# Optimization experiments

Hardware: AMD Instinct MI355X
Metric: run time of the kernel (lower is better)

## Reference

```python
import jax, jax.numpy as jnp
import numpy as np

EPS = 1e-15

def _sqn(x):
    return jnp.sum(x * x, axis=-1, keepdims=True)

def _nrm(x):
    return jnp.sqrt(jnp.clip(_sqn(x), EPS))

def artanh(x):
    return jnp.arctanh(jnp.clip(x, -1 + 1e-7, 1 - 1e-7))

def project(x):
    n = _nrm(x)
    mx = 1.0 - 1e-5
    return jnp.where(n > mx, x / n * mx, x)

def mobius_add(x, y):
    x2, y2 = _sqn(x), _sqn(y)
    xy = jnp.sum(x * y, -1, keepdims=True)
    num = (1 + 2 * xy + y2) * x + (1 - x2) * y
    den = 1 + 2 * xy + x2 * y2
    return num / jnp.clip(den, EPS)

def expmap0(u):
    n = _nrm(u)
    return project(jnp.tanh(n) * u / n)

def logmap0(x):
    n = _nrm(x)
    return artanh(n) * x / n

def pdist(x, y):
    return 2.0 * artanh(_nrm(mobius_add(-x, y)))[..., 0]

def mobius_matvec(x, W):
    # x [..., din], W [din, dout]
    xn = _nrm(x)
    mx = x @ W
    mxn = _nrm(mx)
    return project(jnp.tanh(mxn / xn * artanh(xn)) * mx / mxn)

def mobius_pw_mul(w, x):
    xn = _nrm(x)
    wx = w * x
    wxn = _nrm(wx)
    return project(jnp.tanh(wxn / xn * artanh(xn)) * wx / wxn)

def mobius_linear(x, W, b, nonlin=None):
    out = project(mobius_add(mobius_matvec(x, W), b))
    if nonlin is not None:
        out = project(expmap0(nonlin(logmap0(out))))
    return out

def poincare_to_klein(x):
    return 2 * x / (1 + _sqn(x))

def klein_to_poincare(k):
    return k / (1 + jnp.sqrt(jnp.clip(1 - _sqn(k), EPS)))

def weighted_mobius_midpoint(values, weights):
    # values [..., L, d], weights [..., L, 1]; gyromidpoint via Klein model
    kl = poincare_to_klein(values)
    gamma = 1.0 / jnp.sqrt(jnp.clip(1 - _sqn(kl), EPS))
    num = jnp.sum(weights * gamma * kl, axis=-2)
    den = jnp.sum(weights * gamma, axis=-2)
    return klein_to_poincare(num / jnp.clip(den, EPS))

def mobius_gru(x_seq, Wih, Whh, bias):
    # x_seq [L,B,din]; Wih [3H,din]; Whh [3H,H]; bias [3,H] (points on ball)
    H = Whh.shape[1]
    W_ir, W_ihh, W_iz = jnp.split(Wih, 3, axis=0)
    W_hr, W_hhh, W_hz = jnp.split(Whh, 3, axis=0)
    b_r, b_h, b_z = bias[0], bias[1], bias[2]
    def one_tf(W, h, U, x, b):
        return mobius_add(mobius_add(mobius_matvec(h, W.T), mobius_matvec(x, U.T)), b)
    def step(h, x):
        z = jax.nn.sigmoid(logmap0(one_tf(W_hz, h, W_iz, x, b_z)))
        r = jax.nn.sigmoid(logmap0(one_tf(W_hr, h, W_ir, x, b_r)))
        rh = mobius_pw_mul(r, h)
        h_tilde = one_tf(W_hhh, rh, W_ihh, x, b_h)
        delta = mobius_add(-h, h_tilde)
        hn = mobius_add(h, mobius_pw_mul(z, delta))
        return hn, hn
    h0 = jnp.zeros((x_seq.shape[1], H), x_seq.dtype)
    return jax.lax.scan(step, h0, x_seq)[1]  # [L,B,H]

def mobius_rnn(x_seq, W, U, b):
    # x_seq [L,B,d]; W [d,d] hidden->hidden, U [d,d] input->hidden
    def step(h, x):
        hn = project(mobius_add(mobius_add(mobius_matvec(h, W), mobius_matvec(x, U)), b))
        return hn, hn
    h0 = jnp.zeros(x_seq.shape[1:], x_seq.dtype)
    return jax.lax.scan(step, h0, x_seq)[1]

def distance_attention(values, pos_idx, pos_embeds, Wq, bq, Wk, bk, beta):
    # values [B,L,d], pos_idx [B,L] int
    pe = pos_embeds[pos_idx]
    attn_emb = mobius_add(values, pe)
    q = mobius_linear(attn_emb, Wq, bq)
    k = mobius_linear(attn_emb, Wk, bk)
    d = pdist(q, k)                      # [B,L]
    w = jax.nn.softmax(-beta * d, axis=1)
    return weighted_mobius_midpoint(values, w[..., None]), w

def _forward(context, ctx_position, mentions, mention_chars,
             word_lut, char_lut,
             gru_f_Wih, gru_f_Whh, gru_f_b, gru_b_Wih, gru_b_Whh, gru_b_b,
             w2s_W, w2s_b,
             men_pos, men_Wq, men_bq, men_Wk, men_bk, men_beta,
             char_W, char_U, char_b,
             cc_Wa, cc_Wb, cc_bias,
             ctx_pos, ctx_Wq, ctx_bq, ctx_Wk, ctx_bk, ctx_beta,
             fc_Wm, fc_Wc, fc_Wch, fc_bias,
             mlr_p, mlr_a):
    # ---- mention encoder ----
    men_emb = word_lut[mentions]                                   # B x ML x E
    mv = mobius_linear(men_emb, w2s_W, w2s_b, nonlin=jnp.tanh)     # B x ML x 2S
    ML = mentions.shape[1]
    pos_idx = jnp.where(mentions > 0, jnp.arange(1, ML + 1)[None, :], 0)
    mention_vec, _ = distance_attention(mv, pos_idx, men_pos, men_Wq, men_bq, men_Wk, men_bk, men_beta)
    ch = char_lut[mention_chars]                                   # B x CL x S
    char_states = mobius_rnn(ch.transpose(1, 0, 2), char_W, char_U, char_b).transpose(1, 0, 2)
    char_vec = weighted_mobius_midpoint(char_states, jnp.ones_like(char_states[..., :1]))
    # ---- context encoder (bi-directional hyperbolic GRU) ----
    fwd_emb = word_lut[context].transpose(1, 0, 2)                 # L x B x E
    bkwd_emb = word_lut[context[:, ::-1]].transpose(1, 0, 2)
    fwd_states = mobius_gru(fwd_emb, gru_f_Wih, gru_f_Whh, gru_f_b).transpose(1, 0, 2)
    bkwd_states = mobius_gru(bkwd_emb, gru_b_Wih, gru_b_Whh, gru_b_b).transpose(1, 0, 2)[:, ::-1]
    # ---- mobius concat of directions ----
    ctx = project(mobius_add(mobius_add(mobius_matvec(fwd_states, cc_Wa), mobius_matvec(bkwd_states, cc_Wb)), cc_bias))
    ctx_vec, _ = distance_attention(ctx, ctx_position, ctx_pos, ctx_Wq, ctx_bq, ctx_Wk, ctx_bk, ctx_beta)
    # ---- full mobius concat ----
    joint = mobius_add(mobius_matvec(mention_vec, fc_Wm), mobius_matvec(ctx_vec, fc_Wc))
    joint = project(mobius_add(mobius_add(joint, mobius_matvec(char_vec, fc_Wch)), fc_bias))
    # ---- hyperbolic MLR ----
    z = mobius_add(-mlr_p[None], joint[:, None])                   # B x C x D
    a_n = jnp.sqrt(jnp.clip(jnp.sum(mlr_a * mlr_a, -1), EPS))      # C
    num = 2 * jnp.einsum('bcd,cd->bc', z, mlr_a)
    den = jnp.clip(1 - jnp.sum(z * z, -1), EPS) * a_n
    return 2 * a_n * jnp.arcsinh(num / den)                        # B x C

def setup_inputs() -> dict:
    key = jax.random.key(0)
    ks = iter(jax.random.split(key, 64))
    B, L, ML, CL = 256, 128, 8, 16
    V, CV, E, S, C = 50000, 128, 300, 256, 128
    S2, D = 2 * 256, 5 * 256
    POS_CTX = 2 * 64 + 2  # context_len*2+2
    def u(k, shape, a):
        return jax.random.uniform(k, shape, jnp.float32, -a, a)
    def ball(k, shape, a=1e-4):
        return expmap0(u(k, shape, a))
    def wmat(k, din, dout):
        return u(k, (din, dout), 1.0 / np.sqrt(din))
    inp = {}
    inp['context'] = jax.random.randint(next(ks), (B, L), 0, V)
    inp['ctx_position'] = jax.random.randint(next(ks), (B, L), 0, POS_CTX)
    inp['mentions'] = jax.random.randint(next(ks), (B, ML), 0, V)
    inp['mention_chars'] = jax.random.randint(next(ks), (B, CL), 0, CV)
    inp['word_lut'] = ball(next(ks), (V, E))
    inp['char_lut'] = ball(next(ks), (CV, S))
    for pre in ('gru_f', 'gru_b'):
        inp[pre + '_Wih'] = u(next(ks), (3 * S, E), 1.0 / np.sqrt(S))
        inp[pre + '_Whh'] = u(next(ks), (3 * S, S), 1.0 / np.sqrt(S))
        inp[pre + '_b'] = ball(next(ks), (3, S))
    inp['w2s_W'] = wmat(next(ks), E, S2)
    inp['w2s_b'] = ball(next(ks), (S2,))
    inp['men_pos'] = ball(next(ks), (ML + 1, S2))
    inp['men_Wq'] = wmat(next(ks), S2, S2)
    inp['men_bq'] = ball(next(ks), (S2,))
    inp['men_Wk'] = wmat(next(ks), S2, S2)
    inp['men_bk'] = ball(next(ks), (S2,))
    inp['men_beta'] = u(next(ks), (1,), 0.01)
    inp['char_W'] = wmat(next(ks), S, S)
    inp['char_U'] = wmat(next(ks), S, S)
    inp['char_b'] = ball(next(ks), (S,))
    inp['cc_Wa'] = wmat(next(ks), S, S2)
    inp['cc_Wb'] = wmat(next(ks), S, S2)
    inp['cc_bias'] = ball(next(ks), (S2,))
    inp['ctx_pos'] = ball(next(ks), (POS_CTX, S2))
    inp['ctx_Wq'] = wmat(next(ks), S2, S2)
    inp['ctx_bq'] = ball(next(ks), (S2,))
    inp['ctx_Wk'] = wmat(next(ks), S2, S2)
    inp['ctx_bk'] = ball(next(ks), (S2,))
    inp['ctx_beta'] = u(next(ks), (1,), 0.01)
    inp['fc_Wm'] = wmat(next(ks), S2, D)
    inp['fc_Wc'] = wmat(next(ks), S2, D)
    inp['fc_Wch'] = wmat(next(ks), S, D)
    inp['fc_bias'] = ball(next(ks), (D,))
    inp['mlr_p'] = ball(next(ks), (C, D))
    inp['mlr_a'] = u(next(ks), (C, D), 1.0 / np.sqrt(D))
    return inp

def reference(context, ctx_position, mentions, mention_chars,
              word_lut, char_lut,
              gru_f_Wih, gru_f_Whh, gru_f_b, gru_b_Wih, gru_b_Whh, gru_b_b,
              w2s_W, w2s_b,
              men_pos, men_Wq, men_bq, men_Wk, men_bk, men_beta,
              char_W, char_U, char_b,
              cc_Wa, cc_Wb, cc_bias,
              ctx_pos, ctx_Wq, ctx_bq, ctx_Wk, ctx_bk, ctx_beta,
              fc_Wm, fc_Wc, fc_Wch, fc_bias,
              mlr_p, mlr_a):
    return _forward(context, ctx_position, mentions, mention_chars,
                    word_lut, char_lut,
                    gru_f_Wih, gru_f_Whh, gru_f_b, gru_b_Wih, gru_b_Whh, gru_b_b,
                    w2s_W, w2s_b,
                    men_pos, men_Wq, men_bq, men_Wk, men_bk, men_beta,
                    char_W, char_U, char_b,
                    cc_Wa, cc_Wb, cc_bias,
                    ctx_pos, ctx_Wq, ctx_bq, ctx_Wk, ctx_bk, ctx_beta,
                    fc_Wm, fc_Wc, fc_Wch, fc_bias,
                    mlr_p, mlr_a)
```

## Files before the change

### kernel.cpp

```cpp
#include <hip/hip_runtime.h>
#include <cstddef>
#include <cstdint>


#define EPS_  1e-15f
#define PMAX_ 0.99999f

typedef __attribute__((ext_vector_type(8))) short bf16x8;
typedef __attribute__((ext_vector_type(4))) float f32x4;
typedef __attribute__((ext_vector_type(8))) unsigned short us8;

__device__ __forceinline__ float wred(float v){
#pragma unroll
  for (int o = 32; o; o >>= 1) v += __shfl_xor(v, o, 64);
  return v;
}
__device__ __forceinline__ void wred2(float& a, float& b){
#pragma unroll
  for (int o = 32; o; o >>= 1){ a += __shfl_xor(a, o, 64); b += __shfl_xor(b, o, 64); }
}
__device__ __forceinline__ void wred3(float& a, float& b, float& c){
#pragma unroll
  for (int o = 32; o; o >>= 1){
    a += __shfl_xor(a, o, 64); b += __shfl_xor(b, o, 64); c += __shfl_xor(c, o, 64);
  }
}
__device__ __forceinline__ void wred4(float& a, float& b, float& c, float& d){
#pragma unroll
  for (int o = 32; o; o >>= 1){
    a += __shfl_xor(a, o, 64); b += __shfl_xor(b, o, 64);
    c += __shfl_xor(c, o, 64); d += __shfl_xor(d, o, 64);
  }
}
__device__ __forceinline__ float wredmax(float v){
#pragma unroll
  for (int o = 32; o; o >>= 1) v = fmaxf(v, __shfl_xor(v, o, 64));
  return v;
}
__device__ __forceinline__ float snorm(float s){ return sqrtf(fmaxf(s, EPS_)); }
__device__ __forceinline__ float clamp11(float x){
  return fminf(fmaxf(x, -1.f + 1e-7f), 1.f - 1e-7f);
}
__device__ __forceinline__ float bf2f(unsigned short u){
  union { unsigned int i; float f; } v; v.i = ((unsigned int)u) << 16; return v.f;
}
__device__ __forceinline__ unsigned short f2bf(float f){
  union { float f; unsigned int i; } v; v.f = f;
  unsigned int x = v.i;
  x += 0x7fffu + ((x >> 16) & 1u);
  return (unsigned short)(x >> 16);
}
__device__ __forceinline__ float bflo(unsigned u){
  union { unsigned i; float f; } v; v.i = u << 16; return v.f;
}
__device__ __forceinline__ float bfhi(unsigned u){
  union { unsigned i; float f; } v; v.i = u & 0xffff0000u; return v.f;
}

template<int N>
__device__ __forceinline__ float sq_part(const float* a){
  float s = 0.f;
#pragma unroll
  for (int i = 0; i < N; i++) s += a[i]*a[i];
  return s;
}
template<int N>
__device__ __forceinline__ float dot_part(const float* a, const float* b){
  float s = 0.f;
#pragma unroll
  for (int i = 0; i < N; i++) s += a[i]*b[i];
  return s;
}
template<int N>
__device__ __forceinline__ void madd_vec(const float* x, float x2, const float* y,
                                         float y2, float xy, float* o){
  const float c1 = 1.f + 2.f*xy + y2;
  const float c2 = 1.f - x2;
  const float inv = 1.f / fmaxf(1.f + 2.f*xy + x2*y2, EPS_);
#pragma unroll
  for (int i = 0; i < N; i++) o[i] = (c1*x[i] + c2*y[i]) * inv;
}
template<int N>
__device__ __forceinline__ void mt_project(float* v, float mxn2, float xn2, float* n2out){
  const float xn  = snorm(xn2);
  const float mxn = snorm(mxn2);
  const float t   = tanhf(mxn/xn * atanhf(clamp11(xn)));
  float sc = t/mxn;
  float n2 = sc*sc*mxn2;
  const float n = snorm(n2);
  if (n > PMAX_){ const float s = PMAX_/n; sc *= s; n2 *= s*s; }
#pragma unroll
  for (int i = 0; i < N; i++) v[i] *= sc;
  *n2out = n2;
}
__device__ __forceinline__ void mt_scale(float mxn2, float xn, float art,
                                         float* sc, float* n2){
  const float mxn = snorm(mxn2);
  const float t   = tanhf(mxn/xn * art);
  float s  = t/mxn;
  float nn = t*t;
  const float n = snorm(nn);
  if (n > PMAX_){ const float f = PMAX_/n; s *= f; nn *= f*f; }
  *sc = s; *n2 = nn;
}
template<int N>
__device__ __forceinline__ void project_vec(float* v, float* n2io){
  float n2 = *n2io;
  const float n = snorm(n2);
  if (n > PMAX_){
    const float s = PMAX_/n;
#pragma unroll
    for (int i = 0; i < N; i++) v[i] *= s;
    n2 *= s*s;
  }
  *n2io = n2;
}

__device__ __forceinline__ void gll16(const void* g, void* l){
  __builtin_amdgcn_global_load_lds(
      (const __attribute__((address_space(1))) void*)g,
      (__attribute__((address_space(3))) void*)l, 16, 0, 0);
}
__device__ __forceinline__ void stage64k8(const void* gsrc, float* lbase, int w, int lane){
#pragma unroll
  for (int i = 0; i < 8; i++){
    const char* g = (const char*)gsrc + (size_t)((i*8 + w)*64 + lane)*16;
    char* l = (char*)lbase + (size_t)((i*8 + w)*64)*16;
    gll16(g, l);
  }
}

template<int AMODE>
__global__ __launch_bounds__(256) void mfma_mm(const void* __restrict__ Aptr,
    const int* __restrict__ idx, const unsigned short* __restrict__ Bt,
    float* __restrict__ Cm, int M, int N, int K, int Kp)
{
  __shared__ __align__(16) unsigned short As[128][40];
  __shared__ __align__(16) unsigned short Bs[128][40];
  const int tid = threadIdx.x;
  const int n0 = blockIdx.x * 128;
  const int m0 = blockIdx.y * 128;
  const int srow = tid >> 1, shalf = tid & 1;
  const int wv = tid >> 6, lane = tid & 63;
  const int wm = wv >> 1, wn = wv & 1;
  const int lr = lane & 15, lk = lane >> 4;

  long arow;
  if constexpr (AMODE == 1) arow = (long)idx[m0 + srow] * K;
  else                      arow = (long)(m0 + srow) * K;

  f32x4 acc[4][4];
#pragma unroll
  for (int mf = 0; mf < 4; mf++)
#pragma unroll
    for (int nf = 0; nf < 4; nf++) acc[mf][nf] = (f32x4){0.f,0.f,0.f,0.f};

  for (int k0 = 0; k0 < Kp; k0 += 32){
    const int kb = k0 + shalf*16;
    unsigned short av[16];
    if constexpr (AMODE == 1){
      const float* ar = (const float*)Aptr + arow;
      if (kb + 16 <= K){
#pragma unroll
        for (int v = 0; v < 4; v++){
          const float4 f = *(const float4*)(ar + kb + v*4);
          av[v*4+0]=f2bf(f.x); av[v*4+1]=f2bf(f.y);
          av[v*4+2]=f2bf(f.z); av[v*4+3]=f2bf(f.w);
        }
      } else {
#pragma unroll
        for (int v = 0; v < 16; v++){
          const int col = kb + v;
          av[v] = (col < K) ? f2bf(ar[col]) : (unsigned short)0;
        }
      }
    } else {
      const unsigned short* ar = (const unsigned short*)Aptr + arow + kb;
      const us8 u0 = *(const us8*)ar;
      const us8 u1 = *(const us8*)(ar + 8);
#pragma unroll
      for (int v = 0; v < 8; v++){ av[v] = u0[v]; av[8+v] = u1[v]; }
    }
    unsigned short bvv[16];
    {
      const unsigned short* br = Bt + (long)(n0 + srow)*Kp + kb;
      const us8 u0 = *(const us8*)br;
      const us8 u1 = *(const us8*)(br + 8);
#pragma unroll
      for (int v = 0; v < 8; v++){ bvv[v] = u0[v]; bvv[8+v] = u1[v]; }
    }
    __syncthreads();
    *(us8*)&As[srow][shalf*16]   = *(const us8*)&av[0];
    *(us8*)&As[srow][shalf*16+8] = *(const us8*)&av[8];
    *(us8*)&Bs[srow][shalf*16]   = *(const us8*)&bvv[0];
    *(us8*)&Bs[srow][shalf*16+8] = *(const us8*)&bvv[8];
    __syncthreads();
    bf16x8 af[4], bfr[4];
#pragma unroll
    for (int mf = 0; mf < 4; mf++)
      af[mf] = *(const bf16x8*)&As[wm*64 + mf*16 + lr][lk*8];
#pragma unroll
    for (int nf = 0; nf < 4; nf++)
      bfr[nf] = *(const bf16x8*)&Bs[wn*64 + nf*16 + lr][lk*8];
#pragma unroll
    for (int mf = 0; mf < 4; mf++)
#pragma unroll
      for (int nf = 0; nf < 4; nf++)
        acc[mf][nf] = __builtin_amdgcn_mfma_f32_16x16x32_bf16(af[mf], bfr[nf],
                                                              acc[mf][nf], 0, 0, 0);
  }
#pragma unroll
  for (int mf = 0; mf < 4; mf++){
#pragma unroll
    for (int nf = 0; nf < 4; nf++){
#pragma unroll
      for (int r = 0; r < 4; r++){
        const long grow = m0 + wm*64 + mf*16 + lk*4 + r;
        Cm[grow*N + n0 + wn*64 + nf*16 + lr] = acc[mf][nf][r];
      }
    }
  }
}

template<int AMODE>
__global__ __launch_bounds__(256) void mm_kernel(const void* __restrict__ Aptr,
    const int* __restrict__ idx, const float* __restrict__ Bm,
    float* __restrict__ Cm, int M, int N, int K)
{
  __shared__ __align__(16) float As[8][128];
  __shared__ __align__(16) float Bs[8][132];
  const int tid = threadIdx.x;
  const int n0 = blockIdx.x * 128;
  const int m0 = blockIdx.y * 128;
  const int tr = tid >> 4, tc = tid & 15;
  const int sm = tid & 127, sk = (tid >> 7) * 4;
  const int bk = tid >> 5,  bn = (tid & 31) * 4;
  long arow;
  if constexpr (AMODE == 1) arow = (long)idx[m0 + sm] * K;
  else                      arow = (long)(m0 + sm) * K;
  float acc[8][8];
#pragma unroll
  for (int i = 0; i < 8; i++)
#pragma unroll
    for (int j = 0; j < 8; j++) acc[i][j] = 0.f;

  for (int k0 = 0; k0 < K; k0 += 8){
    float av[4], bv[4];
    {
      const float* A = (const float*)Aptr;
      if (k0 + sk + 3 < K){
        const float4 f = *reinterpret_cast<const float4*>(A + arow + k0 + sk);
        av[0]=f.x; av[1]=f.y; av[2]=f.z; av[3]=f.w;
      } else {
#pragma unroll
        for (int i = 0; i < 4; i++){
          const int kk = k0 + sk + i;
          av[i] = (kk < K) ? A[arow + kk] : 0.f;
        }
      }
    }
    {
      const int kb = k0 + bk;
      if (kb < K){
        const float4 f = *reinterpret_cast<const float4*>(Bm + (long)kb*N + n0 + bn);
        bv[0]=f.x; bv[1]=f.y; bv[2]=f.z; bv[3]=f.w;
      } else { bv[0]=bv[1]=bv[2]=bv[3]=0.f; }
    }
    __syncthreads();
    As[sk+0][sm]=av[0]; As[sk+1][sm]=av[1]; As[sk+2][sm]=av[2]; As[sk+3][sm]=av[3];
    *reinterpret_cast<float4*>(&Bs[bk][bn]) = make_float4(bv[0],bv[1],bv[2],bv[3]);
    __syncthreads();
#pragma unroll
    for (int k = 0; k < 8; k++){
      float a[8], bb[8];
      *(float4*)&a[0]  = *(const float4*)&As[k][tr*8];
      *(float4*)&a[4]  = *(const float4*)&As[k][tr*8+4];
      *(float4*)&bb[0] = *(const float4*)&Bs[k][tc*8];
      *(float4*)&bb[4] = *(const float4*)&Bs[k][tc*8+4];
#pragma unroll
      for (int i = 0; i < 8; i++)
#pragma unroll
        for (int j = 0; j < 8; j++) acc[i][j] += a[i]*bb[j];
    }
  }
#pragma unroll
  for (int i = 0; i < 8; i++){
    const long row = m0 + tr*8 + i;
    *(float4*)(Cm + row*N + n0 + tc*8)     = make_float4(acc[i][0],acc[i][1],acc[i][2],acc[i][3]);
    *(float4*)(Cm + row*N + n0 + tc*8 + 4) = make_float4(acc[i][4],acc[i][5],acc[i][6],acc[i][7]);
  }
}

__global__ __launch_bounds__(256) void transpose_k(const float* __restrict__ src,
    float* __restrict__ dst, int R, int Kc)
{
  __shared__ float t[32][33];
  const int bx = blockIdx.x * 32;
  const int by = blockIdx.y * 32;
  const int tx = threadIdx.x & 31, ty = threadIdx.x >> 5;
#pragma unroll
  for (int i = 0; i < 32; i += 8){
    const int j = by + ty + i, k = bx + tx;
    t[ty+i][tx] = (j < R && k < Kc) ? src[(long)j*Kc + k] : 0.f;
  }
  __syncthreads();
#pragma unroll
  for (int i = 0; i < 32; i += 8){
    const int k = bx + ty + i, j = by + tx;
    if (k < Kc && j < R) dst[(long)k*R + j] = t[tx][ty+i];
  }
}

__global__ __launch_bounds__(256) void packT16(const float* __restrict__ src,
    unsigned short* __restrict__ dst, int K, int N, int Kp)
{
  __shared__ float t[32][33];
  const int bx = blockIdx.x*32;
  const int by = blockIdx.y*32;
  const int tx = threadIdx.x & 31, ty = threadIdx.x >> 5;
#pragma unroll
  for (int i = 0; i < 32; i += 8){
    const int k = bx + ty + i, n = by + tx;
    t[ty+i][tx] = (k < K && n < N) ? src[(long)k*N + n] : 0.f;
  }
  __syncthreads();
#pragma unroll
  for (int i = 0; i < 32; i += 8){
    const int k = bx + tx, n = by + ty + i;
    if (k < Kp && n < N) dst[(long)n*Kp + k] = f2bf(t[tx][ty+i]);
  }
}

__global__ void pack_wih(const float* __restrict__ w0, const float* __restrict__ w1,
                         unsigned short* __restrict__ dst)
{
  const int tid = blockIdx.x*256 + threadIdx.x;
  if (tid < 2*768*320){
    const int d = tid / (768*320);
    const int rem = tid - d*768*320;
    const int n = rem / 320, k = rem - n*320;
    const float* src = d ? w1 : w0;
    dst[tid] = (k < 300) ? f2bf(src[n*300 + k]) : (unsigned short)0;
  }
}

__global__ void pack_whh16(const float* __restrict__ WtHH,
                           unsigned short* __restrict__ Wrz16,
                           unsigned short* __restrict__ Wh16)
{
  const int tid = blockIdx.x*256 + threadIdx.x;
  if (tid < 2*256*768){
    const int col = tid % 768, rk = tid / 768;
    const unsigned short v = f2bf(WtHH[tid]);
    if (col < 256)       Wrz16[(long)rk*512 + col] = v;
    else if (col < 512)  Wh16 [(long)rk*256 + (col - 256)] = v;
    else                 Wrz16[(long)rk*512 + 256 + (col - 512)] = v;
  }
}

__global__ void build_idx(const int* __restrict__ context, const int* __restrict__ mchars,
                          int* __restrict__ ctxidx, int* __restrict__ chidx)
{
  const int tid = blockIdx.x*256 + threadIdx.x;
  if (tid < 32768){
    const int t = tid >> 8, b = tid & 255;
    ctxidx[tid] = context[b*128 + t];
  } else if (tid < 32768 + 4096){
    const int o = tid - 32768;
    const int t = o >> 8, b = o & 255;
    chidx[o] = mchars[b*16 + t];
  }
}

__global__ __launch_bounds__(256) void sqn_gather(const float* __restrict__ lut,
    const int* __restrict__ idx, int K, float* __restrict__ outp)
{
  const int wv = threadIdx.x >> 6, lane = threadIdx.x & 63;
  const int r = blockIdx.x*4 + wv;
  const float* row = lut + (long)idx[r]*K;
  float s = 0.f;
  for (int k = lane; k < K; k += 64) s += row[k]*row[k];
  s = wred(s);
  if (lane == 0) outp[r] = s;
}

__global__ __launch_bounds__(256) void xg_transform(const float* __restrict__ mx,
    const float* __restrict__ xsqn, unsigned short* __restrict__ outp,
    float* __restrict__ n2o, int G)
{
  const int wv = threadIdx.x >> 6, lane = threadIdx.x & 63;
  const int wg = blockIdx.x*4 + wv;
  const int row = wg / G, g = wg - row*G;
  const long base = (long)row*(G*256) + g*256;
  float M[4];
#pragma unroll
  for (int i = 0; i < 4; i++) M[i] = mx[base + i*64 + lane];
  const float mxn2 = wred(sq_part<4>(M));
  float pn2; mt_project<4>(M, mxn2, xsqn[row], &pn2);
  float s = 0.f;
#pragma unroll
  for (int i = 0; i < 4; i++){
    const unsigned short u = f2bf(M[i]);
    outp[base + i*64 + lane] = u;
    const float rv = bf2f(u);
    s += rv*rv;
  }
  s = wred(s);
  if (lane == 0) n2o[wg] = s;
}

#define GRU_LDS_BYTES 153664

__global__ __launch_bounds__(512,1) void gru_kernel(
    const unsigned short* __restrict__ xg,
    const float* __restrict__ xgn2,
    const unsigned short* __restrict__ Wrz16,
    const unsigned short* __restrict__ Wh16,
    const float* __restrict__ bias_f, const float* __restrict__ bias_b,
    unsigned short* __restrict__ states_f, unsigned short* __restrict__ states_b)
{
  extern __shared__ __align__(16) char smem[];
  float* wbuf = (float*)smem;
  float* hs   = (float*)(smem + 131072);
  float* part = (float*)(smem + 133120);
  float* rhb  = (float*)(smem + 149504);
  float* zb   = (float*)(smem + 151552);
  float* scal = (float*)(smem + 153600);

  const int bid = blockIdx.x;
  const int dir = bid >> 7;
  const int brow0 = (bid & 127) * 2;
  const int tid = threadIdx.x;
  const int w = tid >> 6, lane = tid & 63;
  const int j0 = lane << 2;

  const unsigned short* xgd = xg + (long)dir*32768*768;
  const float* xnd = xgn2 + (long)dir*32768*3;
  const unsigned short* wrz_d = Wrz16 + (long)dir*256*512;
  const unsigned short* wh_d  = Wh16  + (long)dir*256*256;
  const float* bias = dir ? bias_b : bias_f;
  unsigned short* states = dir ? states_b : states_f;

  const int fg  = w & 1;
  const int kq4 = w >> 1;
  const int qk8 = w;
  const int crow  = (w >> 1) & 1;
  const int cgate = w & 1;

  float bg[4], bh4[4] = {0,0,0,0};
  float bg2, bh2 = 0.f;
#pragma unroll
  for (int i = 0; i < 4; i++) bg[i] = bias[(cgate ? 512 : 0) + j0 + i];
  bg2 = wred(sq_part<4>(bg));
  if (w < 2){
#pragma unroll
    for (int i = 0; i < 4; i++) bh4[i] = bias[256 + j0 + i];
    bh2 = wred(sq_part<4>(bh4));
  }

  float h[4] = {0.f,0.f,0.f,0.f};
  float hn2 = 0.f;
  if (w < 2){
#pragma unroll
    for (int i = 0; i < 4; i++) hs[w*256 + j0 + i] = 0.f;
    if (lane == 0){ scal[w*2 + 0] = 0.f; scal[w*2 + 1] = 0.f; }
  }

  int cb = 0;
  stage64k8(wrz_d, wbuf, w, lane);

  for (int t = 0; t < 128; t++){
    const int tt = dir ? (127 - t) : t;
    float xgv[4] = {0,0,0,0}, y2g = 0.f, xgh4[4] = {0,0,0,0}, y2h = 0.f;
    if (w < 4){
      const long rxg = (long)tt*256 + brow0 + crow;
      const ushort4 u = *(const ushort4*)(xgd + rxg*768 + (cgate ? 512 : 0) + j0);
      xgv[0]=bf2f(u.x); xgv[1]=bf2f(u.y); xgv[2]=bf2f(u.z); xgv[3]=bf2f(u.w);
      y2g = xnd[rxg*3 + (cgate ? 2 : 0)];
      if (w < 2){
        const long rxh = (long)tt*256 + brow0 + w;
        const ushort4 uh = *(const ushort4*)(xgd + rxh*768 + 256 + j0);
        xgh4[0]=bf2f(uh.x); xgh4[1]=bf2f(uh.y); xgh4[2]=bf2f(uh.z); xgh4[3]=bf2f(uh.w);
        y2h = xnd[rxh*3 + 1];
      }
    }

    float s00=0.f,s01=0.f,s02=0.f,s03=0.f, s10=0.f,s11=0.f,s12=0.f,s13=0.f;
#pragma unroll 1
    for (int c = 0; c < 4; c++){
      __syncthreads();
      if (c < 3) stage64k8((const char*)wrz_d + (size_t)(c+1)*65536,
                           wbuf + (cb^1)*16384, w, lane);
      const uint2* wb2 = (const uint2*)(wbuf + cb*16384);
      const int kb = c*64 + kq4*16;
#pragma unroll
      for (int kk = 0; kk < 4; kk++){
        const float4 hb0 = *(const float4*)&hs[0*256 + kb + kk*4];
        const float4 hb1 = *(const float4*)&hs[1*256 + kb + kk*4];
#pragma unroll
        for (int q = 0; q < 4; q++){
          const uint2 wvv = wb2[(kq4*16 + kk*4 + q)*128 + fg*64 + lane];
          const float w0 = bflo(wvv.x), w1 = bfhi(wvv.x);
          const float w2 = bflo(wvv.y), w3 = bfhi(wvv.y);
          const float h0 = (&hb0.x)[q], h1 = (&hb1.x)[q];
          s00 += h0*w0; s01 += h0*w1; s02 += h0*w2; s03 += h0*w3;
          s10 += h1*w0; s11 += h1*w1; s12 += h1*w2; s13 += h1*w3;
        }
      }
      cb ^= 1;
    }
    {
      float* p1 = part + kq4*1024 + fg*256 + j0;
      *(float4*)p1         = make_float4(s00,s01,s02,s03);
      *(float4*)(p1 + 512) = make_float4(s10,s11,s12,s13);
    }
    __syncthreads();
    stage64k8(wh_d, wbuf + (cb^1)*16384, w, lane);
    cb ^= 1;

    if (w < 4){
      const float* pa = part + crow*512 + cgate*256 + j0;
      const float4 a0 = *(const float4*)pa;
      const float4 a1 = *(const float4*)(pa + 1024);
      const float4 a2 = *(const float4*)(pa + 2048);
      const float4 a3 = *(const float4*)(pa + 3072);
      float a[4] = { (a0.x+a1.x)+(a2.x+a3.x), (a0.y+a1.y)+(a2.y+a3.y),
                     (a0.z+a1.z)+(a2.z+a3.z), (a0.w+a1.w)+(a2.w+a3.w) };
      const float hn2v = scal[crow*2 + 0];
      const float xn_h = snorm(hn2v), art_h = atanhf(clamp11(xn_h));
      const float p2 = wred(sq_part<4>(a));
      float sc, n2; mt_scale(p2, xn_h, art_h, &sc, &n2);
#pragma unroll
      for (int i = 0; i < 4; i++) a[i] *= sc;
      const float xy = wred(dot_part<4>(a, xgv));
      float m1[4]; madd_vec<4>(a, n2, xgv, y2g, xy, m1);
      float m1n2 = sq_part<4>(m1), xyb = dot_part<4>(m1, bg);
      wred2(m1n2, xyb);
      float m2[4]; madd_vec<4>(m1, m1n2, bg, bg2, xyb, m2);
      const float m2n2 = wred(sq_part<4>(m2));
      const float nn = snorm(m2n2), fgc = atanhf(clamp11(nn))/nn;
      float g4[4];
#pragma unroll
      for (int i = 0; i < 4; i++) g4[i] = 1.f/(1.f + expf(-fgc*m2[i]));
      if (cgate == 0){
        float h4[4];
        *(float4*)h4 = *(const float4*)&hs[crow*256 + j0];
        float rh[4]; float wx2 = 0.f;
#pragma unroll
        for (int i = 0; i < 4; i++){ rh[i] = g4[i]*h4[i]; wx2 += rh[i]*rh[i]; }
        wx2 = wred(wx2);
        float rhn2, scrh;
        {
          const float wxn = snorm(wx2);
          const float trh = tanhf(wxn/xn_h * art_h);
          scrh = trh/wxn; rhn2 = trh*trh;
          const float n = snorm(rhn2);
          if (n > PMAX_){ const float f = PMAX_/n; scrh *= f; rhn2 *= f*f; }
        }
#pragma unroll
        for (int i = 0; i < 4; i++) rh[i] *= scrh;
        *(float4*)&rhb[crow*256 + j0] = make_float4(rh[0],rh[1],rh[2],rh[3]);
        if (lane == 0) scal[crow*2 + 1] = rhn2;
      } else {
        *(float4*)&zb[crow*256 + j0] = make_float4(g4[0],g4[1],g4[2],g4[3]);
      }
    }

    float r00=0.f,r01=0.f,r02=0.f,r03=0.f, r10=0.f,r11=0.f,r12=0.f,r13=0.f;
#pragma unroll 1
    for (int c = 0; c < 2; c++){
      __syncthreads();
      if (c < 1) stage64k8((const char*)wh_d + 65536, wbuf + (cb^1)*16384, w, lane);
      const uint2* wb2 = (const uint2*)(wbuf + cb*16384);
      const int kb = c*128 + qk8*16;
#pragma unroll
      for (int kk = 0; kk < 4; kk++){
        const float4 hb0 = *(const float4*)&rhb[0*256 + kb + kk*4];
        const float4 hb1 = *(const float4*)&rhb[1*256 + kb + kk*4];
#pragma unroll
        for (int q = 0; q < 4; q++){
          const uint2 wvv = wb2[(qk8*16 + kk*4 + q)*64 + lane];
          const float w0 = bflo(wvv.x), w1 = bfhi(wvv.x);
          const float w2 = bflo(wvv.y), w3 = bfhi(wvv.y);
          const float h0 = (&hb0.x)[q], h1 = (&hb1.x)[q];
          r00 += h0*w0; r01 += h0*w1; r02 += h0*w2; r03 += h0*w3;
          r10 += h1*w0; r11 += h1*w1; r12 += h1*w2; r13 += h1*w3;
        }
      }
      cb ^= 1;
    }
    {
      float* p2 = part + qk8*512 + j0;
      *(float4*)p2         = make_float4(r00,r01,r02,r03);
      *(float4*)(p2 + 256) = make_float4(r10,r11,r12,r13);
    }
    __syncthreads();
    if (t < 127){
      stage64k8(wrz_d, wbuf + (cb^1)*16384, w, lane);
      cb ^= 1;
    }

    if (w < 2){
      float ah[4];
      {
        float4 p[8];
#pragma unroll
        for (int q = 0; q < 8; q++)
          p[q] = *(const float4*)(part + q*512 + w*256 + j0);
        ah[0] = ((p[0].x+p[1].x)+(p[2].x+p[3].x)) + ((p[4].x+p[5].x)+(p[6].x+p[7].x));
        ah[1] = ((p[0].y+p[1].y)+(p[2].y+p[3].y)) + ((p[4].y+p[5].y)+(p[6].y+p[7].y));
        ah[2] = ((p[0].z+p[1].z)+(p[2].z+p[3].z)) + ((p[4].z+p[5].z)+(p[6].z+p[7].z));
        ah[3] = ((p[0].w+p[1].w)+(p[2].w+p[3].w)) + ((p[4].w+p[5].w)+(p[6].w+p[7].w));
      }
      const float rhn2v = scal[w*2 + 1];
      const float rxn = snorm(rhn2v), artr = atanhf(clamp11(rxn));
      float mx2 = sq_part<4>(ah), xyraw = dot_part<4>(ah, xgh4);
      wred2(mx2, xyraw);
      float sch, pn2; mt_scale(mx2, rxn, artr, &sch, &pn2);
#pragma unroll
      for (int i = 0; i < 4; i++) ah[i] *= sch;
      const float xy = xyraw * sch;
      float m1[4]; madd_vec<4>(ah, pn2, xgh4, y2h, xy, m1);
      float m1n2 = sq_part<4>(m1), xyb = dot_part<4>(m1, bh4);
      wred2(m1n2, xyb);
      float ht[4]; madd_vec<4>(m1, m1n2, bh4, bh2, xyb, ht);
      float htn2 = sq_part<4>(ht);
      float nh[4];
#pragma unroll
      for (int i = 0; i < 4; i++) nh[i] = -h[i];
      float xyd = dot_part<4>(nh, ht);
      wred2(htn2, xyd);
      float dl[4]; madd_vec<4>(nh, hn2, ht, htn2, xyd, dl);
      float z4[4];
      *(float4*)z4 = *(const float4*)&zb[w*256 + j0];
      float pw[4]; float dln2 = 0.f, wz2 = 0.f, xyhr = 0.f;
#pragma unroll
      for (int i = 0; i < 4; i++){
        dln2 += dl[i]*dl[i];
        pw[i] = z4[i]*dl[i];
        wz2  += pw[i]*pw[i];
        xyhr += h[i]*pw[i];
      }
      wred3(dln2, wz2, xyhr);
      float pwn2, scpw;
      {
        const float dn   = snorm(dln2);
        const float artd = atanhf(clamp11(dn));
        const float wzn  = snorm(wz2);
        const float tpw  = tanhf(wzn/dn * artd);
        scpw = tpw/wzn; pwn2 = tpw*tpw;
        const float n = snorm(pwn2);
        if (n > PMAX_){ const float f = PMAX_/n; scpw *= f; pwn2 *= f*f; }
      }
#pragma unroll
      for (int i = 0; i < 4; i++) pw[i] *= scpw;
      const float xyh = xyhr * scpw;
      float hnew[4]; madd_vec<4>(h, hn2, pw, pwn2, xyh, hnew);
#pragma unroll
      for (int i = 0; i < 4; i++) h[i] = hnew[i];
      hn2 = wred(sq_part<4>(h));
      *(float4*)&hs[w*256 + j0] = make_float4(h[0],h[1],h[2],h[3]);
      if (lane == 0) scal[w*2 + 0] = hn2;
      unsigned short* srow = states + ((long)(brow0 + w)*128 + tt)*256 + j0;
      ushort4 su; su.x=f2bf(h[0]); su.y=f2bf(h[1]); su.z=f2bf(h[2]); su.w=f2bf(h[3]);
      *(ushort4*)srow = su;
    }
  }
}

__global__ __launch_bounds__(256) void char_rnn(
    const unsigned short* __restrict__ xgc,
    const float* __restrict__ Wc,
    const float* __restrict__ cb,
    float* __restrict__ cstates)
{
  const int wv = threadIdx.x >> 6, lane = threadIdx.x & 63;
  const int b = blockIdx.x*4 + wv;
  const int j0 = lane << 2;
  __shared__ __align__(16) float hs[4][256];
  float h[4] = {0.f,0.f,0.f,0.f};
  float hn2 = 0.f;
#pragma unroll
  for (int i = 0; i < 4; i++) hs[wv][j0+i] = 0.f;
  float cbv[4];
#pragma unroll
  for (int i = 0; i < 4; i++) cbv[i] = cb[j0+i];
  const float cb2 = wred(sq_part<4>(cbv));
  for (int t = 0; t < 16; t++){
    __syncthreads();
    const unsigned short* xr = xgc + ((long)t*256 + b)*256;
    float xgv[4];
    { const ushort4 u = *(const ushort4*)(xr + j0); xgv[0]=bf2f(u.x); xgv[1]=bf2f(u.y); xgv[2]=bf2f(u.z); xgv[3]=bf2f(u.w); }
    float a[4]={0.f,0.f,0.f,0.f};
#pragma unroll 2
    for (int k0 = 0; k0 < 256; k0 += 4){
      const float4 hk = *(const float4*)&hs[wv][k0];
#pragma unroll
      for (int kk = 0; kk < 4; kk++){
        const float hv = (&hk.x)[kk];
        const float4 w4 = *(const float4*)(Wc + (long)(k0+kk)*256 + j0);
        a[0] += hv*w4.x; a[1] += hv*w4.y; a[2] += hv*w4.z; a[3] += hv*w4.w;
      }
    }
    const float mxn2 = wred(sq_part<4>(a));
    float pn2; mt_project<4>(a, mxn2, hn2, &pn2);
    const float y2 = wred(sq_part<4>(xgv));
    const float xy = wred(dot_part<4>(a, xgv));
    float m1[4]; madd_vec<4>(a, pn2, xgv, y2, xy, m1);
    const float m1n2 = wred(sq_part<4>(m1));
    const float xyb  = wred(dot_part<4>(m1, cbv));
    float m2[4]; madd_vec<4>(m1, m1n2, cbv, cb2, xyb, m2);
    float m2n2 = wred(sq_part<4>(m2));
    project_vec<4>(m2, &m2n2);
#pragma unroll
    for (int i = 0; i < 4; i++) h[i] = m2[i];
    hn2 = m2n2;
    *(float4*)&hs[wv][j0] = make_float4(h[0],h[1],h[2],h[3]);
    *(float4*)(cstates + ((long)b*16 + t)*256 + j0) = make_float4(h[0],h[1],h[2],h[3]);
  }
}

__global__ __launch_bounds__(256) void cc_rowwise(const unsigned short* __restrict__ sf,
    const unsigned short* __restrict__ sb, const float* __restrict__ mxa,
    const float* __restrict__ mxb, const float* __restrict__ ccb,
    unsigned short* __restrict__ ctxo, int rowoff)
{
  const int wv = threadIdx.x >> 6, lane = threadIdx.x & 63;
  const int rloc = blockIdx.x*4 + wv;
  const long r = rowoff + rloc;
  float s = 0.f;
#pragma unroll
  for (int i = 0; i < 4; i++){ const float v = bf2f(sf[r*256 + i*64+lane]); s += v*v; }
  const float sfn2 = wred(s);
  s = 0.f;
#pragma unroll
  for (int i = 0; i < 4; i++){ const float v = bf2f(sb[r*256 + i*64+lane]); s += v*v; }
  const float sbn2 = wred(s);
  float A[8], Bv[8];
#pragma unroll
  for (int i = 0; i < 8; i++){ A[i]  = mxa[(long)rloc*512 + i*64+lane];
                               Bv[i] = mxb[(long)rloc*512 + i*64+lane]; }
  float pan2, pbn2;
  { const float n2 = wred(sq_part<8>(A));  mt_project<8>(A,  n2, sfn2, &pan2); }
  { const float n2 = wred(sq_part<8>(Bv)); mt_project<8>(Bv, n2, sbn2, &pbn2); }
  const float xy = wred(dot_part<8>(A, Bv));
  float M1[8]; madd_vec<8>(A, pan2, Bv, pbn2, xy, M1);
  const float m1n2 = wred(sq_part<8>(M1));
  float Cb[8];
#pragma unroll
  for (int i = 0; i < 8; i++) Cb[i] = ccb[i*64+lane];
  const float cb2 = wred(sq_part<8>(Cb));
  const float xyb = wred(dot_part<8>(M1, Cb));
  float M2[8]; madd_vec<8>(M1, m1n2, Cb, cb2, xyb, M2);
  float m2n2 = wred(sq_part<8>(M2));
  project_vec<8>(M2, &m2n2);
#pragma unroll
  for (int i = 0; i < 8; i++) ctxo[r*512 + i*64+lane] = f2bf(M2[i]);
}

__global__ __launch_bounds__(256) void attn_add(const unsigned short* __restrict__ ctxv,
    const int* __restrict__ pos, const float* __restrict__ pet,
    unsigned short* __restrict__ oemb, float* __restrict__ osqn)
{
  const int wv = threadIdx.x >> 6, lane = threadIdx.x & 63;
  const long r = blockIdx.x*4 + wv;
  float X[8];
#pragma unroll
  for (int i = 0; i < 8; i++) X[i] = bf2f(ctxv[r*512 + i*64+lane]);
  const float x2 = wred(sq_part<8>(X));
  const int p = pos[r];
  float Y[8];
#pragma unroll
  for (int i = 0; i < 8; i++) Y[i] = pet[(long)p*512 + i*64+lane];
  const float y2 = wred(sq_part<8>(Y));
  const float xy = wred(dot_part<8>(X, Y));
  float O[8]; madd_vec<8>(X, x2, Y, y2, xy, O);
  float s = 0.f;
#pragma unroll
  for (int i = 0; i < 8; i++){
    const unsigned short u = f2bf(O[i]);
    oemb[r*512 + i*64+lane] = u;
    const float rv = bf2f(u);
    s += rv*rv;
  }
  s = wred(s);
  if (lane == 0) osqn[r] = s;
}

__global__ __launch_bounds__(256) void attn_add_m(const float* __restrict__ mvv,
    const int* __restrict__ mentions, const float* __restrict__ pet,
    unsigned short* __restrict__ oemb, float* __restrict__ osqn)
{
  const int wv = threadIdx.x >> 6, lane = threadIdx.x & 63;
  const long r = blockIdx.x*4 + wv;
  float X[8];
#pragma unroll
  for (int i = 0; i < 8; i++) X[i] = mvv[r*512 + i*64+lane];
  const float x2 = wred(sq_part<8>(X));
  const int men = mentions[r];
  const int p = (men > 0) ? (int)(r & 7) + 1 : 0;
  float Y[8];
#pragma unroll
  for (int i = 0; i < 8; i++) Y[i] = pet[(long)p*512 + i*64+lane];
  const float y2 = wred(sq_part<8>(Y));
  const float xy = wred(dot_part<8>(X, Y));
  float O[8]; madd_vec<8>(X, x2, Y, y2, xy, O);
  float s = 0.f;
#pragma unroll
  for (int i = 0; i < 8; i++){
    const unsigned short u = f2bf(O[i]);
    oemb[r*512 + i*64+lane] = u;
    const float rv = bf2f(u);
    s += rv*rv;
  }
  s = wred(s);
  if (lane == 0) osqn[r] = s;
}

__global__ __launch_bounds__(256) void qk_pdist(const float* __restrict__ mxq,
    const float* __restrict__ mxk, const float* __restrict__ sqn,
    const float* __restrict__ bq, const float* __restrict__ bk,
    float* __restrict__ dout)
{
  const int wv = threadIdx.x >> 6, lane = threadIdx.x & 63;
  const int r = blockIdx.x*4 + wv;
  const float xn2 = sqn[r];
  float Q[8];
#pragma unroll
  for (int i = 0; i < 8; i++) Q[i] = mxq[(long)r*512 + i*64+lane];
  { const float n2 = wred(sq_part<8>(Q)); float pn2; mt_project<8>(Q, n2, xn2, &pn2);
    float Bq[8];
#pragma unroll
    for (int i = 0; i < 8; i++) Bq[i] = bq[i*64+lane];
    const float b2 = wred(sq_part<8>(Bq));
    const float xy = wred(dot_part<8>(Q, Bq));
    float O[8]; madd_vec<8>(Q, pn2, Bq, b2, xy, O);
#pragma unroll
    for (int i = 0; i < 8; i++) Q[i] = O[i];
  }
  float qn2 = wred(sq_part<8>(Q));
  project_vec<8>(Q, &qn2);
  float Kv[8];
#pragma unroll
  for (int i = 0; i < 8; i++) Kv[i] = mxk[(long)r*512 + i*64+lane];
  { const float n2 = wred(sq_part<8>(Kv)); float pn2; mt_project<8>(Kv, n2, xn2, &pn2);
    float Bk[8];
#pragma unroll
    for (int i = 0; i < 8; i++) Bk[i] = bk[i*64+lane];
    const float b2 = wred(sq_part<8>(Bk));
    const float xy = wred(dot_part<8>(Kv, Bk));
    float O[8]; madd_vec<8>(Kv, pn2, Bk, b2, xy, O);
#pragma unroll
    for (int i = 0; i < 8; i++) Kv[i] = O[i];
  }
  float kn2 = wred(sq_part<8>(Kv));
  project_vec<8>(Kv, &kn2);
  float NQ[8];
#pragma unroll
  for (int i = 0; i < 8; i++) NQ[i] = -Q[i];
  const float xy = wred(dot_part<8>(NQ, Kv));
  float Z[8]; madd_vec<8>(NQ, qn2, Kv, kn2, xy, Z);
  const float zn2 = wred(sq_part<8>(Z));
  const float d = 2.f * atanhf(clamp11(snorm(zn2)));
  if (lane == 0) dout[r] = d;
}

__global__ __launch_bounds__(256) void softmax128(const float* __restrict__ d,
    const float* __restrict__ beta, float* __restrict__ w)
{
  const int wv = threadIdx.x >> 6, lane = threadIdx.x & 63;
  const int b = blockIdx.x*4 + wv;
  const float bt = beta[0];
  const float x0 = -bt * d[b*128 + lane];
  const float x1 = -bt * d[b*128 + 64 + lane];
  const float m = wredmax(fmaxf(x0, x1));
  const float e0 = expf(x0 - m), e1 = expf(x1 - m);
  const float s = wred(e0 + e1);
  w[b*128 + lane]      = e0 / s;
  w[b*128 + 64 + lane] = e1 / s;
}

__global__ void softmax8(const float* __restrict__ d, const float* __restrict__ beta,
                         float* __restrict__ w)
{
  const int b = threadIdx.x;
  const float bt = beta[0];
  float x[8]; float m = -1e30f;
#pragma unroll
  for (int i = 0; i < 8; i++){ x[i] = -bt * d[b*8+i]; m = fmaxf(m, x[i]); }
  float s = 0.f;
#pragma unroll
  for (int i = 0; i < 8; i++){ x[i] = expf(x[i]-m); s += x[i]; }
#pragma unroll
  for (int i = 0; i < 8; i++) w[b*8+i] = x[i] / s;
}

template<int NPL, bool BF16V, bool HASW>
__global__ __launch_bounds__(256) void midpoint_kernel(const void* __restrict__ vals,
    const float* __restrict__ wts, float* __restrict__ outp, int Lseq)
{
  const int wv = threadIdx.x >> 6, lane = threadIdx.x & 63;
  const int b = blockIdx.x*4 + wv;
  const int D = NPL*64;
  float num[NPL];
#pragma unroll
  for (int i = 0; i < NPL; i++) num[i] = 0.f;
  float den = 0.f;
  for (int l = 0; l < Lseq; l++){
    const long base = ((long)b*Lseq + l)*D;
    float v[NPL]; float s = 0.f;
#pragma unroll
    for (int i = 0; i < NPL; i++){
      v[i] = BF16V ? bf2f(((const unsigned short*)vals)[base + i*64+lane])
                   : ((const float*)vals)[base + i*64+lane];
      s += v[i]*v[i];
    }
    const float v2 = wred(s);
    const float f = 2.f/(1.f + v2);
    const float kl2 = v2*f*f;
    const float gamma = 1.f/sqrtf(fmaxf(1.f - kl2, EPS_));
    const float wgt = HASW ? wts[b*Lseq + l] : 1.f;
    const float wg = wgt*gamma;
#pragma unroll
    for (int i = 0; i < NPL; i++) num[i] += wg*(f*v[i]);
    den += wg;
  }
  den = fmaxf(den, EPS_);
  float x[NPL]; float s = 0.f;
#pragma unroll
  for (int i = 0; i < NPL; i++){ x[i] = num[i]/den; s += x[i]*x[i]; }
  const float k2 = wred(s);
  const float inv = 1.f/(1.f + sqrtf(fmaxf(1.f - k2, EPS_)));
#pragma unroll
  for (int i = 0; i < NPL; i++) outp[(long)b*D + i*64+lane] = x[i]*inv;
}

__global__ __launch_bounds__(512) void midpoint_wide(
    const unsigned short* __restrict__ vals,
    const float* __restrict__ wts,
    float* __restrict__ outp)
{
  __shared__ float pnum[8][512];
  __shared__ float pden[8];
  __shared__ float red[512];
  __shared__ float kk2[1];
  const int b = blockIdx.x;
  const int tid = threadIdx.x;
  const int w = tid >> 6, lane = tid & 63;
  float num[8] = {0.f,0.f,0.f,0.f,0.f,0.f,0.f,0.f};
  float den = 0.f;
  for (int l = w; l < 128; l += 8){
    const long base = ((long)b*128 + l)*512;
    float v[8]; float s = 0.f;
#pragma unroll
    for (int i = 0; i < 8; i++){
      v[i] = bf2f(vals[base + i*64 + lane]);
      s += v[i]*v[i];
    }
    const float v2 = wred(s);
    const float f = 2.f/(1.f + v2);
    const float kl2 = v2*f*f;
    const float gamma = 1.f/sqrtf(fmaxf(1.f - kl2, EPS_));
    const float wg = wts[b*128 + l]*gamma;
#pragma unroll
    for (int i = 0; i < 8; i++) num[i] += wg*(f*v[i]);
    den += wg;
  }
#pragma unroll
  for (int i = 0; i < 8; i++) pnum[w][i*64 + lane] = num[i];
// ... 316 lines not shown
```

Before: 2.807 ms.

## Deepen GRU weight staging to a 4-slot ring with explicit vmcnt waits

Weight streaming in the recurrent GRU kernel changes from double-buffered 64KB chunks to a four-slot ring of 32KB chunks with three chunks in flight. Waits use explicit s_waitcnt vmcnt and raw barriers, and prefetch runs across the r/z and h phases and into the next timestep. The aim is to hide global-to-LDS load latency that the old per-chunk __syncthreads serialized. In exchange there is more barrier traffic per step and fragile hand-written wait counts that must match outstanding loads exactly.

Result: slower. 3.002 ms (+6.9%).

```diff
diff --git a/kernel.cpp b/kernel.cpp
--- a/kernel.cpp
+++ b/kernel.cpp
@@ -9,6 +9,12 @@
 typedef __attribute__((ext_vector_type(8))) short bf16x8;
 typedef __attribute__((ext_vector_type(4))) float f32x4;
 typedef __attribute__((ext_vector_type(8))) unsigned short us8;
+
+#define WAITC8 asm volatile("s_waitcnt vmcnt(8)" ::: "memory")
+#define WAITC4 asm volatile("s_waitcnt vmcnt(4)" ::: "memory")
+#define WAITC0 asm volatile("s_waitcnt vmcnt(0)" ::: "memory")
+#define LGKM0  asm volatile("s_waitcnt lgkmcnt(0)" ::: "memory")
+#define BARR   do{ __builtin_amdgcn_s_barrier(); __builtin_amdgcn_sched_barrier(0); }while(0)
 
 __device__ __forceinline__ float wred(float v){
 #pragma unroll
@@ -121,9 +127,9 @@
       (const __attribute__((address_space(1))) void*)g,
       (__attribute__((address_space(3))) void*)l, 16, 0, 0);
 }
-__device__ __forceinline__ void stage64k8(const void* gsrc, float* lbase, int w, int lane){
-#pragma unroll
-  for (int i = 0; i < 8; i++){
+__device__ __forceinline__ void stage32k8(const void* gsrc, float* lbase, int w, int lane){
+#pragma unroll
+  for (int i = 0; i < 4; i++){
     const char* g = (const char*)gsrc + (size_t)((i*8 + w)*64 + lane)*16;
     char* l = (char*)lbase + (size_t)((i*8 + w)*64)*16;
     gll16(g, l);
@@ -465,10 +471,13 @@
     for (int i = 0; i < 4; i++) hs[w*256 + j0 + i] = 0.f;
     if (lane == 0){ scal[w*2 + 0] = 0.f; scal[w*2 + 1] = 0.f; }
   }
-
-  int cb = 0;
-  stage64k8(wrz_d, wbuf, w, lane);
-
+  __syncthreads();
+
+  stage32k8(wrz_d,           wbuf + 0*8192, w, lane);
+  stage32k8(wrz_d + 16384,   wbuf + 1*8192, w, lane);
+  stage32k8(wrz_d + 2*16384, wbuf + 2*8192, w, lane);
+
+#pragma unroll 1
   for (int t = 0; t < 128; t++){
     const int tt = dir ? (127 - t) : t;
     float xgv[4] = {0,0,0,0}, y2g = 0.f, xgh4[4] = {0,0,0,0}, y2h = 0.f;
@@ -487,19 +496,24 @@
 
     float s00=0.f,s01=0.f,s02=0.f,s03=0.f, s10=0.f,s11=0.f,s12=0.f,s13=0.f;
 #pragma unroll 1
-    for (int c = 0; c < 4; c++){
-      __syncthreads();
-      if (c < 3) stage64k8((const char*)wrz_d + (size_t)(c+1)*65536,
-                           wbuf + (cb^1)*16384, w, lane);
-      const uint2* wb2 = (const uint2*)(wbuf + cb*16384);
-      const int kb = c*64 + kq4*16;
-#pragma unroll
-      for (int kk = 0; kk < 4; kk++){
+    for (int c = 0; c < 8; c++){
+      WAITC8;
+      BARR;
+      {
+        const int is = c + 3;
+        const unsigned short* src = (is < 8) ? (wrz_d + is*16384)
+                                             : (wh_d + (is - 8)*16384);
+        stage32k8(src, wbuf + (is & 3)*8192, w, lane);
+      }
+      const uint2* wb2 = (const uint2*)(wbuf + (c & 3)*8192);
+      const int kb = c*32 + kq4*8;
+#pragma unroll
+      for (int kk = 0; kk < 2; kk++){
         const float4 hb0 = *(const float4*)&hs[0*256 + kb + kk*4];
         const float4 hb1 = *(const float4*)&hs[1*256 + kb + kk*4];
 #pragma unroll
         for (int q = 0; q < 4; q++){
-          const uint2 wvv = wb2[(kq4*16 + kk*4 + q)*128 + fg*64 + lane];
+          const uint2 wvv = wb2[(kq4*8 + kk*4 + q)*128 + fg*64 + lane];
           const float w0 = bflo(wvv.x), w1 = bfhi(wvv.x);
           const float w2 = bflo(wvv.y), w3 = bfhi(wvv.y);
           const float h0 = (&hb0.x)[q], h1 = (&hb1.x)[q];
@@ -507,16 +521,14 @@
           s10 += h1*w0; s11 += h1*w1; s12 += h1*w2; s13 += h1*w3;
         }
       }
-      cb ^= 1;
     }
     {
       float* p1 = part + kq4*1024 + fg*256 + j0;
       *(float4*)p1         = make_float4(s00,s01,s02,s03);
       *(float4*)(p1 + 512) = make_float4(s10,s11,s12,s13);
     }
-    __syncthreads();
-    stage64k8(wh_d, wbuf + (cb^1)*16384, w, lane);
-    cb ^= 1;
+    LGKM0;
+    BARR;
 
     if (w < 4){
       const float* pa = part + crow*512 + cgate*256 + j0;
@@ -568,18 +580,34 @@
 
     float r00=0.f,r01=0.f,r02=0.f,r03=0.f, r10=0.f,r11=0.f,r12=0.f,r13=0.f;
 #pragma unroll 1
-    for (int c = 0; c < 2; c++){
-      __syncthreads();
-      if (c < 1) stage64k8((const char*)wh_d + 65536, wbuf + (cb^1)*16384, w, lane);
-      const uint2* wb2 = (const uint2*)(wbuf + cb*16384);
-      const int kb = c*128 + qk8*16;
-#pragma unroll
-      for (int kk = 0; kk < 4; kk++){
+    for (int c = 0; c < 4; c++){
+      const int s = 8 + c;
+      if (t < 127){ WAITC8; }
+      else {
+        if      (c <  2){ WAITC8; }
+        else if (c == 2){ WAITC4; }
+        else            { WAITC0; }
+      }
+      if (c == 0){ LGKM0; }
+      BARR;
+      {
+        const int is = s + 3;
+        if (is < 12){
+          stage32k8(wh_d + (is - 8)*16384, wbuf + (is & 3)*8192, w, lane);
+        } else if (t < 127){
+          const int nis = is - 12;
+          stage32k8(wrz_d + nis*16384, wbuf + (nis & 3)*8192, w, lane);
+        }
+      }
+      const uint2* wb2 = (const uint2*)(wbuf + (s & 3)*8192);
+      const int kb = c*64 + qk8*8;
+#pragma unroll
+      for (int kk = 0; kk < 2; kk++){
         const float4 hb0 = *(const float4*)&rhb[0*256 + kb + kk*4];
         const float4 hb1 = *(const float4*)&rhb[1*256 + kb + kk*4];
 #pragma unroll
         for (int q = 0; q < 4; q++){
-          const uint2 wvv = wb2[(qk8*16 + kk*4 + q)*64 + lane];
+          const uint2 wvv = wb2[(qk8*8 + kk*4 + q)*64 + lane];
           const float w0 = bflo(wvv.x), w1 = bfhi(wvv.x);
           const float w2 = bflo(wvv.y), w3 = bfhi(wvv.y);
           const float h0 = (&hb0.x)[q], h1 = (&hb1.x)[q];
@@ -587,18 +615,14 @@
           r10 += h1*w0; r11 += h1*w1; r12 += h1*w2; r13 += h1*w3;
         }
       }
-      cb ^= 1;
     }
     {
       float* p2 = part + qk8*512 + j0;
       *(float4*)p2         = make_float4(r00,r01,r02,r03);
       *(float4*)(p2 + 256) = make_float4(r10,r11,r12,r13);
     }
-    __syncthreads();
-    if (t < 127){
-      stage64k8(wrz_d, wbuf + (cb^1)*16384, w, lane);
-      cb ^= 1;
-    }
+    LGKM0;
+    BARR;
 
     if (w < 2){
       float ah[4];
@@ -665,6 +689,8 @@
       ushort4 su; su.x=f2bf(h[0]); su.y=f2bf(h[1]); su.z=f2bf(h[2]); su.w=f2bf(h[3]);
       *(ushort4*)srow = su;
     }
+    LGKM0;
+    BARR;
   }
 }
 
```
